# Optimization experiments

Measured on AMD Instinct MI355X. Metric: run time of the kernel, lower is better.

Reference implementation:

```python
import jax, jax.numpy as jnp
import numpy as np

N_NODES = 50000
N_EDGES = 300000
INPUT_DIM = 128
HIDDEN_DIM = 256
NUM_HEADS = 8
HEAD_DIM = HIDDEN_DIM // NUM_HEADS  # 32
NUM_EDGE_TYPES = 3


def setup_inputs() -> dict:
    key = jax.random.key(0)
    ks = jax.random.split(key, 12)
    s_in = 1.0 / np.sqrt(INPUT_DIM)
    s_hid = 1.0 / np.sqrt(HIDDEN_DIM)
    return {
        "node_features": jax.random.normal(ks[0], (N_NODES, INPUT_DIM), jnp.float32),
        "edges": jax.random.randint(ks[1], (N_EDGES, 2), 0, N_NODES),
        "edge_types": jax.random.randint(ks[2], (N_EDGES,), 0, NUM_EDGE_TYPES),
        # torch.nn.Linear convention: y = x @ W.T + b, W: [out, in]
        "Wq": jax.random.normal(ks[3], (HIDDEN_DIM, INPUT_DIM), jnp.float32) * s_in,
        "bq": jax.random.normal(ks[4], (HIDDEN_DIM,), jnp.float32) * s_in,
        "Wk": jax.random.normal(ks[5], (HIDDEN_DIM, INPUT_DIM), jnp.float32) * s_in,
        "bk": jax.random.normal(ks[6], (HIDDEN_DIM,), jnp.float32) * s_in,
        "Wv": jax.random.normal(ks[7], (HIDDEN_DIM, INPUT_DIM), jnp.float32) * s_in,
        "bv": jax.random.normal(ks[8], (HIDDEN_DIM,), jnp.float32) * s_in,
        "edge_emb": jax.random.normal(ks[9], (NUM_EDGE_TYPES, HIDDEN_DIM), jnp.float32),
        "Wo": jax.random.normal(ks[10], (INPUT_DIM, HIDDEN_DIM), jnp.float32) * s_hid,
        "bo": jax.random.normal(ks[11], (INPUT_DIM,), jnp.float32) * s_hid,
    }


def reference(node_features, edges, edge_types, Wq, bq, Wk, bk, Wv, bv, edge_emb, Wo, bo):
    # Project all nodes once, split heads: [N, H, D]
    Q = (node_features @ Wq.T + bq).reshape(-1, NUM_HEADS, HEAD_DIM)
    K = (node_features @ Wk.T + bk).reshape(-1, NUM_HEADS, HEAD_DIM)
    V = (node_features @ Wv.T + bv).reshape(-1, NUM_HEADS, HEAD_DIM)

    src = edges[:, 0]
    tgt = edges[:, 1]

    # Per-edge small attention: Q[src] [E,H,D] x K[tgt]^T -> [E,H,H]
    # (identical math to the original per-edge-type loop, since only the
    #  edge embedding depends on edge_type and it is gathered per edge)
    scale = 1.0 / jnp.sqrt(jnp.float32(HEAD_DIM))
    scores = jnp.einsum("ehd,egd->ehg", Q[src], K[tgt]) * scale
    attn = jax.nn.softmax(scores, axis=-1)
    msg = jnp.einsum("ehg,egd->ehd", attn, V[tgt]).reshape(-1, HIDDEN_DIM)  # [E, HID]

    msg = msg + edge_emb[edge_types]          # per-edge-type embedding add
    out_e = msg @ Wo.T + bo                   # output projection per edge [E, IN]

    # Scatter-add over source nodes (original Python loop over edges)
    messages = jax.ops.segment_sum(out_e, src, num_segments=N_NODES)
    return messages
```

## Files before the change

kernel.cpp:

```cpp
#include <hip/hip_runtime.h>

#define N_NODES 50000
#define N_EDGES 300000
#define M_PAD 50048
#define M_PAD2 50176
#define NBLK 196
#define SC 0.17677669529663687f

typedef __attribute__((ext_vector_type(8))) short bf16x8;
typedef __attribute__((ext_vector_type(4))) short bf16x4;
typedef __attribute__((ext_vector_type(4))) float f32x4;

__device__ __forceinline__ unsigned short f2bf(float x) {
    unsigned int u = __float_as_uint(x);
    unsigned int r = (u + 0x7FFFu + ((u >> 16) & 1u)) >> 16;
    return (unsigned short)r;
}

__global__ __launch_bounds__(512)
void qkv_gemm(const unsigned short* __restrict__ A2, const unsigned short* __restrict__ B2,
              const float* __restrict__ biasCat,
              unsigned short* __restrict__ Qb, unsigned short* __restrict__ Kb,
              unsigned short* __restrict__ Vb)
{
    constexpr int K2 = 128;
    const int t    = threadIdx.x;
    const int w    = t >> 6;
    const int lane = t & 63;
    const int l15  = lane & 15;
    const int lg   = lane >> 4;
    const int bx   = blockIdx.x;
    const int m0   = blockIdx.y * 128;
    const int wm   = (w >> 2) * 64;
    const int wn   = (w & 3) * 64;
    const float mulc = (bx == 0) ? SC : 1.0f;

    f32x4 acc[4][4] = {};

    const unsigned short* Abase = A2 + (size_t)(m0 + wm + l15) * K2 + lg * 8;
    const unsigned short* Bbase = B2 + (size_t)(bx * 256 + wn + l15) * K2 + lg * 8;

    #pragma unroll 2
    for (int ks = 0; ks < K2 / 32; ++ks) {
        bf16x8 af[4], bfv[4];
        #pragma unroll
        for (int mi = 0; mi < 4; ++mi)
            af[mi] = *(const bf16x8*)(Abase + (size_t)mi * 16 * K2 + ks * 32);
        #pragma unroll
        for (int ni = 0; ni < 4; ++ni)
            bfv[ni] = *(const bf16x8*)(Bbase + (size_t)ni * 16 * K2 + ks * 32);
        #pragma unroll
        for (int mi = 0; mi < 4; ++mi)
            #pragma unroll
            for (int ni = 0; ni < 4; ++ni)
                acc[mi][ni] = __builtin_amdgcn_mfma_f32_16x16x32_bf16(
                    af[mi], bfv[ni], acc[mi][ni], 0, 0, 0);
    }

    __shared__ unsigned short Cs[64 * 256];
    float bvn[4];
    #pragma unroll
    for (int ni = 0; ni < 4; ++ni)
        bvn[ni] = biasCat[bx * 256 + wn + ni * 16 + l15];

    #pragma unroll
    for (int p = 0; p < 2; ++p) {
        if (p) __syncthreads();
        #pragma unroll
        for (int mi2 = 0; mi2 < 2; ++mi2) {
            const int mi = p * 2 + mi2;
            #pragma unroll
            for (int j = 0; j < 4; ++j) {
                const int lr = (wm >> 1) + mi2 * 16 + lg * 4 + j;
                const int xr = (lr & 7) << 3;
                #pragma unroll
                for (int ni = 0; ni < 4; ++ni) {
                    const int col = wn + ni * 16 + l15;
                    Cs[lr * 256 + (col ^ xr)] = f2bf(fmaf(acc[mi][ni][j], mulc, bvn[ni]));
                }
            }
        }
        __syncthreads();

        if (bx < 2) {
            unsigned short* dst = bx ? Kb : Qb;
            #pragma unroll
            for (int c8 = 0; c8 < 4; ++c8) {
                const int chunk = c8 * 512 + t;
                const int lr = chunk >> 5;
                const int ec = (chunk & 31) * 8;
                const int gr = m0 + ((lr < 32) ? (p * 32 + lr)
                                               : (64 + p * 32 + (lr - 32)));
                const bf16x8 v = *(const bf16x8*)&Cs[lr * 256 + (ec ^ ((lr & 7) << 3))];
                *(bf16x8*)&dst[(size_t)gr * 256 + ec] = v;
            }
        } else {
            #pragma unroll
            for (int c8 = 0; c8 < 4; ++c8) {
                const int chunk = c8 * 512 + t;
                const int lr = chunk >> 5;
                const int ec = (chunk & 31) * 8;
                const int gr = m0 + ((lr < 32) ? (p * 32 + lr)
                                               : (64 + p * 32 + (lr - 32)));
                const int d  = ec >> 3;
                const int xr = (lr & 7) << 3;
                bf16x8 v;
                #pragma unroll
                for (int g = 0; g < 8; ++g)
                    v[g] = (short)Cs[lr * 256 + ((g * 32 + d) ^ xr)];
                *(bf16x8*)&Vb[(size_t)gr * 256 + ec] = v;
            }
        }
    }
}

__global__ __launch_bounds__(128)
void out_gemm(const unsigned short* __restrict__ accQ, const unsigned short* __restrict__ B2o,
              const float* __restrict__ eew, const float* __restrict__ bo,
              const float4* __restrict__ cnt4, float* __restrict__ Cout)
{
    const int t    = threadIdx.x;
    const int w    = t >> 6;
    const int lane = t & 63;
    const int l15  = lane & 15;
    const int lg   = lane >> 4;
    const int m0   = blockIdx.y * 64;
    const int wn   = w * 64;

    f32x4 acc[4][4] = {};

    const unsigned short* Abase = accQ + (size_t)(m0 + l15) * 256 + lg * 8;
    const unsigned short* Bbase = B2o + (size_t)(wn + l15) * 256 + lg * 8;

    #pragma unroll 2
    for (int ks = 0; ks < 8; ++ks) {
        bf16x8 af[4], bfv[4];
        #pragma unroll
        for (int mi = 0; mi < 4; ++mi)
            af[mi] = *(const bf16x8*)(Abase + (size_t)mi * 16 * 256 + ks * 32);
        #pragma unroll
        for (int ni = 0; ni < 4; ++ni)
            bfv[ni] = *(const bf16x8*)(Bbase + (size_t)ni * 16 * 256 + ks * 32);
        #pragma unroll
        for (int mi = 0; mi < 4; ++mi)
            #pragma unroll
            for (int ni = 0; ni < 4; ++ni)
                acc[mi][ni] = __builtin_amdgcn_mfma_f32_16x16x32_bf16(
                    af[mi], bfv[ni], acc[mi][ni], 0, 0, 0);
    }

    #pragma unroll
    for (int mi = 0; mi < 4; ++mi)
        #pragma unroll
        for (int j = 0; j < 4; ++j) {
            const int row = m0 + mi * 16 + lg * 4 + j;
            if (row < N_NODES) {
                const float4 cv = cnt4[row];
                #pragma unroll
                for (int ni = 0; ni < 4; ++ni) {
                    const int col = wn + ni * 16 + l15;
                    Cout[(size_t)row * 128 + col] = acc[mi][ni][j]
                        + cv.x * eew[col] + cv.y * eew[128 + col]
                        + cv.z * eew[256 + col] + cv.w * bo[col];
                }
            }
        }
}

__global__ __launch_bounds__(256)
void conv_nf_kernel(const float4* __restrict__ nf4, unsigned short* __restrict__ A2)
{
    const int tid = blockIdx.x * 256 + threadIdx.x;
    if (tid >= N_NODES * 32) return;
    const int m = tid >> 5, k4 = (tid & 31) * 4;
    const float4 v = nf4[tid];
    ushort4 hi;
    hi.x = f2bf(v.x); hi.y = f2bf(v.y); hi.z = f2bf(v.z); hi.w = f2bf(v.w);
    *reinterpret_cast<ushort4*>(&A2[(size_t)m * 128 + k4]) = hi;
}

__global__ __launch_bounds__(256)
void prep_kernel(const float* __restrict__ Wq, const float* __restrict__ Wk,
                 const float* __restrict__ Wv, const float* __restrict__ bq,
                 const float* __restrict__ bk, const float* __restrict__ bv,
                 const float* __restrict__ Wo, const float* __restrict__ ee,
                 unsigned short* __restrict__ B2qkv, unsigned short* __restrict__ B2o,
                 float* __restrict__ biasCat, float* __restrict__ eew)
{
    const int bid = blockIdx.x, t = threadIdx.x;
    if (bid < 384) {
        const int tid = bid * 256 + t;
        const int r = tid >> 7, k = tid & 127;
        const float* W = (r < 256) ? Wq : (r < 512) ? Wk : Wv;
        B2qkv[(size_t)r * 128 + k] = f2bf(W[(size_t)(r & 255) * 128 + k]);
        if (k == 0) {
            const float* b = (r < 256) ? bq : (r < 512) ? bk : bv;
            biasCat[r] = b[r & 255] * ((r < 256) ? SC : 1.0f);
        }
    } else if (bid < 512) {
        const int tid = (bid - 384) * 256 + t;
        const int r = tid >> 8, k = tid & 255;
        B2o[(size_t)r * 256 + k] = f2bf(Wo[(size_t)r * 256 + k]);
    } else if (t < 128) {
        float a0 = 0.f, a1 = 0.f, a2 = 0.f;
        for (int k = 0; k < 256; ++k) {
            const float w = Wo[(size_t)t * 256 + k];
            a0 += ee[k] * w; a1 += ee[256 + k] * w; a2 += ee[512 + k] * w;
        }
        eew[t] = a0; eew[128 + t] = a1; eew[256 + t] = a2;
    }
}

__global__ __launch_bounds__(256)
void hist_kernel(const int* __restrict__ edges, int* __restrict__ deg)
{
    const int e = blockIdx.x * 256 + threadIdx.x;
    if (e < N_EDGES) atomicAdd(&deg[edges[2 * e]], 1);
}

__global__ __launch_bounds__(256)
void scan_part1(const int* __restrict__ deg, int* __restrict__ blockSum)
{
    const int t = threadIdx.x;
    const int i = blockIdx.x * 256 + t;
    int v = (i < N_NODES) ? deg[i] : 0;
    #pragma unroll
    for (int o = 1; o < 64; o <<= 1) v += __shfl_xor(v, o);
    __shared__ int ws[4];
    if ((t & 63) == 0) ws[t >> 6] = v;
    __syncthreads();
    if (t == 0) blockSum[blockIdx.x] = ws[0] + ws[1] + ws[2] + ws[3];
}

__global__ __launch_bounds__(256)
void scan_part2(const int* __restrict__ blockSum, int* __restrict__ blockBase,
                int* __restrict__ rowStart)
{
    __shared__ int lds[256];
    const int t = threadIdx.x;
    lds[t] = (t < NBLK) ? blockSum[t] : 0;
    __syncthreads();
    #pragma unroll
    for (int o = 1; o < 256; o <<= 1) {
        const int u = (t >= o) ? lds[t - o] : 0;
        __syncthreads();
        lds[t] += u;
        __syncthreads();
    }
    if (t < NBLK) blockBase[t] = (t == 0) ? 0 : lds[t - 1];
    if (t == 0) rowStart[N_NODES] = N_EDGES;
}

__global__ __launch_bounds__(256)
void scan_part3(const int* __restrict__ deg, const int* __restrict__ blockBase,
                int* __restrict__ rowStart, int* __restrict__ cursor)
{
    const int t = threadIdx.x;
    const int lane = t & 63, wid = t >> 6;
    const int i = blockIdx.x * 256 + t;
    const int d = (i < N_NODES) ? deg[i] : 0;
    int x = d;
    #pragma unroll
    for (int o = 1; o < 64; o <<= 1) {
        const int u = __shfl_up(x, o);
        if (lane >= o) x += u;
    }
    __shared__ int wtot[4];
    if (lane == 63) wtot[wid] = x;
    __syncthreads();
    int wo = 0;
    #pragma unroll
    for (int wi = 0; wi < 3; ++wi) wo += (wi < wid) ? wtot[wi] : 0;
    const int excl = blockBase[blockIdx.x] + wo + x - d;
    if (i < N_NODES) { rowStart[i] = excl; cursor[i] = excl; }
}

__global__ __launch_bounds__(256)
void scatter_kernel(const int* __restrict__ edges, const int* __restrict__ etypes,
                    int* __restrict__ cursor, int* __restrict__ packed)
{
    const int e = blockIdx.x * 256 + threadIdx.x;
    if (e < N_EDGES) {
        const int pos = atomicAdd(&cursor[edges[2 * e]], 1);
        packed[pos] = edges[2 * e + 1] | (etypes[e] << 20);
    }
}

__device__ __forceinline__ bf16x4 softmax_pa(f32x4 s, bool valid)
{
    float mx = fmaxf(fmaxf(s[0], s[1]), fmaxf(s[2], s[3]));
    mx = fmaxf(mx, __shfl_xor(mx, 16));
    const float e0 = __expf(s[0] - mx), e1 = __expf(s[1] - mx);
    const float e2 = __expf(s[2] - mx), e3 = __expf(s[3] - mx);
    float sum = e0 + e1 + e2 + e3;
    sum += __shfl_xor(sum, 16);
    const float inv = valid ? (1.0f / sum) : 0.0f;
    bf16x4 pa;
    pa[0] = (short)f2bf(e0 * inv);
    pa[1] = (short)f2bf(e1 * inv);
    pa[2] = (short)f2bf(e2 * inv);
    pa[3] = (short)f2bf(e3 * inv);
    return pa;
}

__global__ __launch_bounds__(256)
void node_gather_kernel(const int* __restrict__ packed, const int* __restrict__ rowStart,
                        const unsigned short* __restrict__ Qb,
                        const unsigned short* __restrict__ Kb,
                        const unsigned short* __restrict__ Vb,
                        unsigned short* __restrict__ accQ, float4* __restrict__ cnt4)
{
    const int lane = threadIdx.x & 63;
    const int n = blockIdx.x * 4 + (threadIdx.x >> 6);
    if (n >= N_NODES) return;
    const int l15 = lane & 15;
    const int lg  = lane >> 4;

    const bf16x8 qf = *(const bf16x8*)&Qb[(size_t)n * 256 + (l15 & 7) * 32 + lg * 8];

    f32x4 cpvA0 = {0.f,0.f,0.f,0.f}, cpvA1 = {0.f,0.f,0.f,0.f};
    f32x4 cpvB0 = {0.f,0.f,0.f,0.f}, cpvB1 = {0.f,0.f,0.f,0.f};
    int cnt = 0;

    const int lo = rowStart[n], hi = rowStart[n + 1];
    const bool validBase = ((l15 < 8) == (lg < 2));
    const f32x4 z4 = {0.f, 0.f, 0.f, 0.f};
    int idx = lo;

    for (; idx + 4 <= hi; idx += 4) {
        const int p0 = packed[idx],     p1 = packed[idx + 1];
        const int p2 = packed[idx + 2], p3 = packed[idx + 3];
        const int t0 = p0 & 0xFFFFF, t1 = p1 & 0xFFFFF;
        const int t2 = p2 & 0xFFFFF, t3 = p3 & 0xFFFFF;
        cnt += (1 << ((p0 >> 20) * 10)) + (1 << ((p1 >> 20) * 10))
             + (1 << ((p2 >> 20) * 10)) + (1 << ((p3 >> 20) * 10));

        const int tkA = (l15 < 8) ? t0 : t1;
        const int tkB = (l15 < 8) ? t2 : t3;
        const bf16x8 kfA = *(const bf16x8*)&Kb[(size_t)tkA * 256 + (l15 & 7) * 32 + lg * 8];
        const bf16x8 kfB = *(const bf16x8*)&Kb[(size_t)tkB * 256 + (l15 & 7) * 32 + lg * 8];

        const int tvA = (lg < 2) ? t0 : t1;
        const int tvB = (lg < 2) ? t2 : t3;
        const unsigned short* vrA = &Vb[(size_t)tvA * 256 + (lg & 1) * 4];
        const unsigned short* vrB = &Vb[(size_t)tvB * 256 + (lg & 1) * 4];
        const bf16x4 vfA0 = *(const bf16x4*)&vrA[l15 * 8];
        const bf16x4 vfA1 = *(const bf16x4*)&vrA[(l15 + 16) * 8];
        const bf16x4 vfB0 = *(const bf16x4*)&vrB[l15 * 8];
        const bf16x4 vfB1 = *(const bf16x4*)&vrB[(l15 + 16) * 8];

        const f32x4 sA = __builtin_amdgcn_mfma_f32_16x16x32_bf16(kfA, qf, z4, 0, 0, 0);
        const f32x4 sB = __builtin_amdgcn_mfma_f32_16x16x32_bf16(kfB, qf, z4, 0, 0, 0);

        const bf16x4 paA = softmax_pa(sA, validBase);
        const bf16x4 paB = softmax_pa(sB, validBase);

        cpvA0 = __builtin_amdgcn_mfma_f32_16x16x16bf16_1k(paA, vfA0, cpvA0, 0, 0, 0);
        cpvA1 = __builtin_amdgcn_mfma_f32_16x16x16bf16_1k(paA, vfA1, cpvA1, 0, 0, 0);
        cpvB0 = __builtin_amdgcn_mfma_f32_16x16x16bf16_1k(paB, vfB0, cpvB0, 0, 0, 0);
        cpvB1 = __builtin_amdgcn_mfma_f32_16x16x16bf16_1k(paB, vfB1, cpvB1, 0, 0, 0);
    }

    for (; idx < hi; idx += 2) {
        const int  p0  = packed[idx];
        const bool dup = (idx + 1 >= hi);
        const int  p1  = dup ? p0 : packed[idx + 1];
        const int  t0  = p0 & 0xFFFFF;
        const int  t1  = p1 & 0xFFFFF;
        cnt += (1 << ((p0 >> 20) * 10));
        if (!dup) cnt += (1 << ((p1 >> 20) * 10));

        const int tk = (l15 < 8) ? t0 : t1;
        const bf16x8 kf = *(const bf16x8*)&Kb[(size_t)tk * 256 + (l15 & 7) * 32 + lg * 8];

        const int tv = (lg < 2) ? t0 : t1;
        const unsigned short* vrow = &Vb[(size_t)tv * 256 + (lg & 1) * 4];
        const bf16x4 vf0 = *(const bf16x4*)&vrow[l15 * 8];
        const bf16x4 vf1 = *(const bf16x4*)&vrow[(l15 + 16) * 8];

        const f32x4 s = __builtin_amdgcn_mfma_f32_16x16x32_bf16(kf, qf, z4, 0, 0, 0);
        const bool valid = validBase && !(dup && (l15 >= 8));
        const bf16x4 pa = softmax_pa(s, valid);

        cpvA0 = __builtin_amdgcn_mfma_f32_16x16x16bf16_1k(pa, vf0, cpvA0, 0, 0, 0);
        cpvA1 = __builtin_amdgcn_mfma_f32_16x16x16bf16_1k(pa, vf1, cpvA1, 0, 0, 0);
    }

    f32x4 cpv0 = cpvA0 + cpvB0;
    f32x4 cpv1 = cpvA1 + cpvB1;

    #pragma unroll
    for (int j = 0; j < 4; ++j) {
        cpv0[j] += __shfl_xor(cpv0[j], 32);
        cpv1[j] += __shfl_xor(cpv1[j], 32);
    }

    if (lane < 32) {
        unsigned short* row = &accQ[(size_t)n * 256];
        #pragma unroll
        for (int j = 0; j < 4; ++j) {
            const int h = lg * 4 + j;
            row[h * 32 + l15]      = f2bf(cpv0[j]);
            row[h * 32 + 16 + l15] = f2bf(cpv1[j]);
        }
    }
    if (lane == 0) {
        const int c0 = cnt & 1023, c1 = (cnt >> 10) & 1023, c2 = (cnt >> 20) & 1023;
        cnt4[n] = make_float4((float)c0, (float)c1, (float)c2, (float)(hi - lo));
    }
}

extern "C" void kernel_launch(void* const* d_in, const int* in_sizes, int n_in,
                              void* d_out, int out_size, void* d_ws, size_t ws_size,
                              hipStream_t stream)
{
    const float* nf      = (const float*)d_in[0];
    const int*   edges   = (const int*)d_in[1];
    const int*   etypes  = (const int*)d_in[2];
    const float* Wq      = (const float*)d_in[3];
    const float* bq      = (const float*)d_in[4];
    const float* Wk      = (const float*)d_in[5];
    const float* bk      = (const float*)d_in[6];
    const float* Wv      = (const float*)d_in[7];
    const float* bv      = (const float*)d_in[8];
    const float* ee      = (const float*)d_in[9];
    const float* Wo      = (const float*)d_in[10];
    const float* bo      = (const float*)d_in[11];
    float* out = (float*)d_out;

    char* ws = (char*)d_ws;
    size_t off = 0;
    auto alloc = [&](size_t bytes) -> void* {
        void* p = ws + off;
        off = (off + bytes + 255) & ~(size_t)255;
        return p;
    };
    unsigned short* A2    = (unsigned short*)alloc((size_t)M_PAD * 128 * 2);
    unsigned short* B2qkv = (unsigned short*)alloc((size_t)768 * 128 * 2);
    unsigned short* B2o   = (unsigned short*)alloc((size_t)128 * 256 * 2);
    float*          biasC = (float*)alloc(768 * sizeof(float));
    float*          eew   = (float*)alloc(384 * sizeof(float));
    unsigned short* Qb    = (unsigned short*)alloc((size_t)M_PAD * 256 * 2);
    unsigned short* Kb    = (unsigned short*)alloc((size_t)M_PAD * 256 * 2);
    unsigned short* Vb    = (unsigned short*)alloc((size_t)M_PAD * 256 * 2);
    unsigned short* accQ  = (unsigned short*)alloc((size_t)M_PAD2 * 256 * 2);
    float4* cnt4 = (float4*)alloc((size_t)N_NODES * sizeof(float4));
    int*    deg  = (int*)alloc((size_t)N_NODES * sizeof(int));
    int*    rowS = (int*)alloc((size_t)(N_NODES + 1) * sizeof(int));
    int*    curs = (int*)alloc((size_t)N_NODES * sizeof(int));
    int*    pck  = (int*)alloc((size_t)N_EDGES * sizeof(int));
    int*    bSum = (int*)alloc((size_t)NBLK * sizeof(int));
    int*    bBase= (int*)alloc((size_t)NBLK * sizeof(int));

    const dim3 blk(256);

    conv_nf_kernel<<<dim3((N_NODES * 32 + 255) / 256), blk, 0, stream>>>((const float4*)nf, A2);
    prep_kernel<<<dim3(513), blk, 0, stream>>>(Wq, Wk, Wv, bq, bk, bv, Wo, ee, B2qkv, B2o, biasC, eew);

    hipMemsetAsync(deg, 0, (size_t)N_NODES * sizeof(int), stream);
    hist_kernel<<<dim3((N_EDGES + 255) / 256), blk, 0, stream>>>(edges, deg);
    scan_part1<<<dim3(NBLK), blk, 0, stream>>>(deg, bSum);
    scan_part2<<<dim3(1), blk, 0, stream>>>(bSum, bBase, rowS);
    scan_part3<<<dim3(NBLK), blk, 0, stream>>>(deg, bBase, rowS, curs);
    scatter_kernel<<<dim3((N_EDGES + 255) / 256), blk, 0, stream>>>(edges, etypes, curs, pck);

    qkv_gemm<<<dim3(3, M_PAD / 128), dim3(512), 0, stream>>>(
        A2, B2qkv, biasC, Qb, Kb, Vb);

    node_gather_kernel<<<dim3((N_NODES + 3) / 4), blk, 0, stream>>>(
        pck, rowS, Qb, Kb, Vb, accQ, cnt4);

    out_gemm<<<dim3(1, M_PAD2 / 64), dim3(128), 0, stream>>>(
        accQ, B2o, eew, bo, cnt4, out);
}
```

Before: 181.8 us.

## Fuse prep kernels, compute per-type edge counts via histogram, drop softmax max

Merges the feature conversion, weight prep and degree histogram into one launch, and makes the histogram count edges per (node, type) so scan_part3 writes cnt4 directly. The gather kernel no longer unpacks edge types or counts them. The softmax max-subtraction is removed and it now uses a fast reciprocal and library bf16 conversion. The output GEMM tile is halved to 32 rows to launch more blocks. Dropping the max-subtraction risks exp overflow when scores are large, and the 4x larger histogram adds memset and atomic traffic.

```diff
diff --git a/kernel.cpp b/kernel.cpp
--- a/kernel.cpp
+++ b/kernel.cpp
@@ -1,4 +1,5 @@
 #include <hip/hip_runtime.h>
+#include <hip/hip_bf16.h>
 
 #define N_NODES 50000
 #define N_EDGES 300000
@@ -7,6 +8,10 @@
 #define NBLK 196
 #define SC 0.17677669529663687f
 
+#define MB_CONV 6250
+#define MB_HIST 1172
+#define MB_PREP 513
+
 typedef __attribute__((ext_vector_type(8))) short bf16x8;
 typedef __attribute__((ext_vector_type(4))) short bf16x4;
 typedef __attribute__((ext_vector_type(4))) float f32x4;
@@ -15,6 +20,10 @@
     unsigned int u = __float_as_uint(x);
     unsigned int r = (u + 0x7FFFu + ((u >> 16) & 1u)) >> 16;
     return (unsigned short)r;
+}
+__device__ __forceinline__ short bfs(float x) {
+    __hip_bfloat16 h = __float2bfloat16(x);
+    return *reinterpret_cast<short*>(&h);
 }
 
 __global__ __launch_bounds__(512)
@@ -124,25 +133,25 @@
     const int lane = t & 63;
     const int l15  = lane & 15;
     const int lg   = lane >> 4;
-    const int m0   = blockIdx.y * 64;
+    const int m0   = blockIdx.y * 32;
     const int wn   = w * 64;
 
-    f32x4 acc[4][4] = {};
+    f32x4 acc[2][4] = {};
 
     const unsigned short* Abase = accQ + (size_t)(m0 + l15) * 256 + lg * 8;
     const unsigned short* Bbase = B2o + (size_t)(wn + l15) * 256 + lg * 8;
 
     #pragma unroll 2
     for (int ks = 0; ks < 8; ++ks) {
-        bf16x8 af[4], bfv[4];
-        #pragma unroll
-        for (int mi = 0; mi < 4; ++mi)
+        bf16x8 af[2], bfv[4];
+        #pragma unroll
+        for (int mi = 0; mi < 2; ++mi)
             af[mi] = *(const bf16x8*)(Abase + (size_t)mi * 16 * 256 + ks * 32);
         #pragma unroll
         for (int ni = 0; ni < 4; ++ni)
             bfv[ni] = *(const bf16x8*)(Bbase + (size_t)ni * 16 * 256 + ks * 32);
         #pragma unroll
-        for (int mi = 0; mi < 4; ++mi)
+        for (int mi = 0; mi < 2; ++mi)
             #pragma unroll
             for (int ni = 0; ni < 4; ++ni)
                 acc[mi][ni] = __builtin_amdgcn_mfma_f32_16x16x32_bf16(
@@ -150,7 +159,7 @@
     }
 
     #pragma unroll
-    for (int mi = 0; mi < 4; ++mi)
+    for (int mi = 0; mi < 2; ++mi)
         #pragma unroll
         for (int j = 0; j < 4; ++j) {
             const int row = m0 + mi * 16 + lg * 4 + j;
@@ -168,62 +177,64 @@
 }
 
 __global__ __launch_bounds__(256)
-void conv_nf_kernel(const float4* __restrict__ nf4, unsigned short* __restrict__ A2)
-{
-    const int tid = blockIdx.x * 256 + threadIdx.x;
-    if (tid >= N_NODES * 32) return;
-    const int m = tid >> 5, k4 = (tid & 31) * 4;
-    const float4 v = nf4[tid];
-    ushort4 hi;
-    hi.x = f2bf(v.x); hi.y = f2bf(v.y); hi.z = f2bf(v.z); hi.w = f2bf(v.w);
-    *reinterpret_cast<ushort4*>(&A2[(size_t)m * 128 + k4]) = hi;
-}
-
-__global__ __launch_bounds__(256)
-void prep_kernel(const float* __restrict__ Wq, const float* __restrict__ Wk,
-                 const float* __restrict__ Wv, const float* __restrict__ bq,
-                 const float* __restrict__ bk, const float* __restrict__ bv,
-                 const float* __restrict__ Wo, const float* __restrict__ ee,
-                 unsigned short* __restrict__ B2qkv, unsigned short* __restrict__ B2o,
-                 float* __restrict__ biasCat, float* __restrict__ eew)
+void mega_prep(const float4* __restrict__ nf4,
+               const int* __restrict__ edges, const int* __restrict__ etypes,
+               const float* __restrict__ Wq, const float* __restrict__ Wk,
+               const float* __restrict__ Wv, const float* __restrict__ bq,
+               const float* __restrict__ bk, const float* __restrict__ bv,
+               const float* __restrict__ Wo, const float* __restrict__ ee,
+               unsigned short* __restrict__ A2, unsigned short* __restrict__ B2qkv,
+               unsigned short* __restrict__ B2o,
+               float* __restrict__ biasCat, float* __restrict__ eew,
+               int* __restrict__ degType)
 {
     const int bid = blockIdx.x, t = threadIdx.x;
-    if (bid < 384) {
+    if (bid < MB_CONV) {
         const int tid = bid * 256 + t;
-        const int r = tid >> 7, k = tid & 127;
-        const float* W = (r < 256) ? Wq : (r < 512) ? Wk : Wv;
-        B2qkv[(size_t)r * 128 + k] = f2bf(W[(size_t)(r & 255) * 128 + k]);
-        if (k == 0) {
-            const float* b = (r < 256) ? bq : (r < 512) ? bk : bv;
-            biasCat[r] = b[r & 255] * ((r < 256) ? SC : 1.0f);
+        const int m = tid >> 5, k4 = (tid & 31) * 4;
+        const float4 v = nf4[tid];
+        ushort4 hi;
+        hi.x = f2bf(v.x); hi.y = f2bf(v.y); hi.z = f2bf(v.z); hi.w = f2bf(v.w);
+        *reinterpret_cast<ushort4*>(&A2[(size_t)m * 128 + k4]) = hi;
+    } else if (bid < MB_CONV + MB_HIST) {
+        const int e = (bid - MB_CONV) * 256 + t;
+        if (e < N_EDGES) atomicAdd(&degType[edges[2 * e] * 4 + etypes[e]], 1);
+    } else {
+        const int pbid = bid - MB_CONV - MB_HIST;
+        if (pbid < 384) {
+            const int tid = pbid * 256 + t;
+            const int r = tid >> 7, k = tid & 127;
+            const float* W = (r < 256) ? Wq : (r < 512) ? Wk : Wv;
+            B2qkv[(size_t)r * 128 + k] = f2bf(W[(size_t)(r & 255) * 128 + k]);
+            if (k == 0) {
+                const float* b = (r < 256) ? bq : (r < 512) ? bk : bv;
+                biasCat[r] = b[r & 255] * ((r < 256) ? SC : 1.0f);
+            }
+        } else if (pbid < 512) {
+            const int tid = (pbid - 384) * 256 + t;
+            const int r = tid >> 8, k = tid & 255;
+            B2o[(size_t)r * 256 + k] = f2bf(Wo[(size_t)r * 256 + k]);
+        } else if (t < 128) {
+            float a0 = 0.f, a1 = 0.f, a2 = 0.f;
+            for (int k = 0; k < 256; ++k) {
+                const float w = Wo[(size_t)t * 256 + k];
+                a0 += ee[k] * w; a1 += ee[256 + k] * w; a2 += ee[512 + k] * w;
+            }
+            eew[t] = a0; eew[128 + t] = a1; eew[256 + t] = a2;
         }
-    } else if (bid < 512) {
-        const int tid = (bid - 384) * 256 + t;
-        const int r = tid >> 8, k = tid & 255;
-        B2o[(size_t)r * 256 + k] = f2bf(Wo[(size_t)r * 256 + k]);
-    } else if (t < 128) {
-        float a0 = 0.f, a1 = 0.f, a2 = 0.f;
-        for (int k = 0; k < 256; ++k) {
-            const float w = Wo[(size_t)t * 256 + k];
-            a0 += ee[k] * w; a1 += ee[256 + k] * w; a2 += ee[512 + k] * w;
-        }
-        eew[t] = a0; eew[128 + t] = a1; eew[256 + t] = a2;
-    }
-}
-
-__global__ __launch_bounds__(256)
-void hist_kernel(const int* __restrict__ edges, int* __restrict__ deg)
-{
-    const int e = blockIdx.x * 256 + threadIdx.x;
-    if (e < N_EDGES) atomicAdd(&deg[edges[2 * e]], 1);
-}
-
-__global__ __launch_bounds__(256)
-void scan_part1(const int* __restrict__ deg, int* __restrict__ blockSum)
+    }
+}
+
+__global__ __launch_bounds__(256)
+void scan_part1(const int4* __restrict__ degType4, int* __restrict__ blockSum)
 {
     const int t = threadIdx.x;
     const int i = blockIdx.x * 256 + t;
-    int v = (i < N_NODES) ? deg[i] : 0;
+    int v = 0;
+    if (i < N_NODES) {
+        const int4 dt = degType4[i];
+        v = dt.x + dt.y + dt.z;
+    }
     #pragma unroll
     for (int o = 1; o < 64; o <<= 1) v += __shfl_xor(v, o);
     __shared__ int ws[4];
@@ -252,13 +263,16 @@
 }
 
 __global__ __launch_bounds__(256)
-void scan_part3(const int* __restrict__ deg, const int* __restrict__ blockBase,
-                int* __restrict__ rowStart, int* __restrict__ cursor)
+void scan_part3(const int4* __restrict__ degType4, const int* __restrict__ blockBase,
+                int* __restrict__ rowStart, int* __restrict__ cursor,
+                float4* __restrict__ cnt4)
 {
     const int t = threadIdx.x;
     const int lane = t & 63, wid = t >> 6;
     const int i = blockIdx.x * 256 + t;
-    const int d = (i < N_NODES) ? deg[i] : 0;
+    int4 dt = make_int4(0, 0, 0, 0);
+    if (i < N_NODES) dt = degType4[i];
+    const int d = dt.x + dt.y + dt.z;
     int x = d;
     #pragma unroll
     for (int o = 1; o < 64; o <<= 1) {
@@ -272,34 +286,36 @@
     #pragma unroll
     for (int wi = 0; wi < 3; ++wi) wo += (wi < wid) ? wtot[wi] : 0;
     const int excl = blockBase[blockIdx.x] + wo + x - d;
-    if (i < N_NODES) { rowStart[i] = excl; cursor[i] = excl; }
-}
-
-__global__ __launch_bounds__(256)
-void scatter_kernel(const int* __restrict__ edges, const int* __restrict__ etypes,
-                    int* __restrict__ cursor, int* __restrict__ packed)
+    if (i < N_NODES) {
+        rowStart[i] = excl;
+        cursor[i]   = excl;
+        cnt4[i]     = make_float4((float)dt.x, (float)dt.y, (float)dt.z, (float)d);
+    }
+}
+
+__global__ __launch_bounds__(256)
+void scatter_kernel(const int* __restrict__ edges, int* __restrict__ cursor,
+                    int* __restrict__ packed)
 {
     const int e = blockIdx.x * 256 + threadIdx.x;
     if (e < N_EDGES) {
         const int pos = atomicAdd(&cursor[edges[2 * e]], 1);
-        packed[pos] = edges[2 * e + 1] | (etypes[e] << 20);
+        packed[pos] = edges[2 * e + 1];
     }
 }
 
 __device__ __forceinline__ bf16x4 softmax_pa(f32x4 s, bool valid)
 {
-    float mx = fmaxf(fmaxf(s[0], s[1]), fmaxf(s[2], s[3]));
-    mx = fmaxf(mx, __shfl_xor(mx, 16));
-    const float e0 = __expf(s[0] - mx), e1 = __expf(s[1] - mx);
-    const float e2 = __expf(s[2] - mx), e3 = __expf(s[3] - mx);
+    const float e0 = __expf(s[0]), e1 = __expf(s[1]);
+    const float e2 = __expf(s[2]), e3 = __expf(s[3]);
     float sum = e0 + e1 + e2 + e3;
     sum += __shfl_xor(sum, 16);
-    const float inv = valid ? (1.0f / sum) : 0.0f;
+    const float inv = valid ? __builtin_amdgcn_rcpf(sum) : 0.0f;
     bf16x4 pa;
-    pa[0] = (short)f2bf(e0 * inv);
-    pa[1] = (short)f2bf(e1 * inv);
-    pa[2] = (short)f2bf(e2 * inv);
-    pa[3] = (short)f2bf(e3 * inv);
+    pa[0] = bfs(e0 * inv);
+    pa[1] = bfs(e1 * inv);
+    pa[2] = bfs(e2 * inv);
+    pa[3] = bfs(e3 * inv);
     return pa;
 }
 
@@ -308,7 +324,7 @@
                         const unsigned short* __restrict__ Qb,
                         const unsigned short* __restrict__ Kb,
                         const unsigned short* __restrict__ Vb,
-                        unsigned short* __restrict__ accQ, float4* __restrict__ cnt4)
+                        unsigned short* __restrict__ accQ)
 {
     const int lane = threadIdx.x & 63;
     const int n = blockIdx.x * 4 + (threadIdx.x >> 6);
@@ -320,7 +336,6 @@
 
     f32x4 cpvA0 = {0.f,0.f,0.f,0.f}, cpvA1 = {0.f,0.f,0.f,0.f};
     f32x4 cpvB0 = {0.f,0.f,0.f,0.f}, cpvB1 = {0.f,0.f,0.f,0.f};
-    int cnt = 0;
 
     const int lo = rowStart[n], hi = rowStart[n + 1];
     const bool validBase = ((l15 < 8) == (lg < 2));
@@ -328,12 +343,8 @@
     int idx = lo;
 
     for (; idx + 4 <= hi; idx += 4) {
-        const int p0 = packed[idx],     p1 = packed[idx + 1];
-        const int p2 = packed[idx + 2], p3 = packed[idx + 3];
-        const int t0 = p0 & 0xFFFFF, t1 = p1 & 0xFFFFF;
-        const int t2 = p2 & 0xFFFFF, t3 = p3 & 0xFFFFF;
-        cnt += (1 << ((p0 >> 20) * 10)) + (1 << ((p1 >> 20) * 10))
-             + (1 << ((p2 >> 20) * 10)) + (1 << ((p3 >> 20) * 10));
+        const int t0 = packed[idx],     t1 = packed[idx + 1];
+        const int t2 = packed[idx + 2], t3 = packed[idx + 3];
 
         const int tkA = (l15 < 8) ? t0 : t1;
         const int tkB = (l15 < 8) ? t2 : t3;
@@ -362,13 +373,9 @@
     }
 
     for (; idx < hi; idx += 2) {
-        const int  p0  = packed[idx];
+        const int  t0  = packed[idx];
         const bool dup = (idx + 1 >= hi);
-        const int  p1  = dup ? p0 : packed[idx + 1];
-        const int  t0  = p0 & 0xFFFFF;
-        const int  t1  = p1 & 0xFFFFF;
-        cnt += (1 << ((p0 >> 20) * 10));
-        if (!dup) cnt += (1 << ((p1 >> 20) * 10));
+        const int  t1  = dup ? t0 : packed[idx + 1];
 
         const int tk = (l15 < 8) ? t0 : t1;
         const bf16x8 kf = *(const bf16x8*)&Kb[(size_t)tk * 256 + (l15 & 7) * 32 + lg * 8];
@@ -400,13 +407,9 @@
         #pragma unroll
         for (int j = 0; j < 4; ++j) {
             const int h = lg * 4 + j;
-            row[h * 32 + l15]      = f2bf(cpv0[j]);
-            row[h * 32 + 16 + l15] = f2bf(cpv1[j]);
+            row[h * 32 + l15]      = (unsigned short)bfs(cpv0[j]);
+            row[h * 32 + 16 + l15] = (unsigned short)bfs(cpv1[j]);
         }
-    }
-    if (lane == 0) {
-        const int c0 = cnt & 1023, c1 = (cnt >> 10) & 1023, c2 = (cnt >> 20) & 1023;
-        cnt4[n] = make_float4((float)c0, (float)c1, (float)c2, (float)(hi - lo));
     }
 }
 
@@ -435,41 +438,41 @@
         off = (off + bytes + 255) & ~(size_t)255;
         return p;
     };
-    unsigned short* A2    = (unsigned short*)alloc((size_t)M_PAD * 128 * 2);
-    unsigned short* B2qkv = (unsigned short*)alloc((size_t)768 * 128 * 2);
-    unsigned short* B2o   = (unsigned short*)alloc((size_t)128 * 256 * 2);
-    float*          biasC = (float*)alloc(768 * sizeof(float));
-    float*          eew   = (float*)alloc(384 * sizeof(float));
-    unsigned short* Qb    = (unsigned short*)alloc((size_t)M_PAD * 256 * 2);
-    unsigned short* Kb    = (unsigned short*)alloc((size_t)M_PAD * 256 * 2);
-    unsigned short* Vb    = (unsigned short*)alloc((size_t)M_PAD * 256 * 2);
-    unsigned short* accQ  = (unsigned short*)alloc((size_t)M_PAD2 * 256 * 2);
-    float4* cnt4 = (float4*)alloc((size_t)N_NODES * sizeof(float4));
-    int*    deg  = (int*)alloc((size_t)N_NODES * sizeof(int));
-    int*    rowS = (int*)alloc((size_t)(N_NODES + 1) * sizeof(int));
-    int*    curs = (int*)alloc((size_t)N_NODES * sizeof(int));
-    int*    pck  = (int*)alloc((size_t)N_EDGES * sizeof(int));
-    int*    bSum = (int*)alloc((size_t)NBLK * sizeof(int));
-    int*    bBase= (int*)alloc((size_t)NBLK * sizeof(int));
+    unsigned short* A2     = (unsigned short*)alloc((size_t)M_PAD * 128 * 2);
+    unsigned short* B2qkv  = (unsigned short*)alloc((size_t)768 * 128 * 2);
+    unsigned short* B2o    = (unsigned short*)alloc((size_t)128 * 256 * 2);
+    float*          biasC  = (float*)alloc(768 * sizeof(float));
+    float*          eew    = (float*)alloc(384 * sizeof(float));
+    unsigned short* Qb     = (unsigned short*)alloc((size_t)M_PAD * 256 * 2);
+    unsigned short* Kb     = (unsigned short*)alloc((size_t)M_PAD * 256 * 2);
+    unsigned short* Vb     = (unsigned short*)alloc((size_t)M_PAD * 256 * 2);
+    unsigned short* accQ   = (unsigned short*)alloc((size_t)M_PAD2 * 256 * 2);
+    float4* cnt4    = (float4*)alloc((size_t)N_NODES * sizeof(float4));
+    int*    degType = (int*)alloc((size_t)N_NODES * 4 * sizeof(int));
+    int*    rowS    = (int*)alloc((size_t)(N_NODES + 1) * sizeof(int));
+    int*    curs    = (int*)alloc((size_t)N_NODES * sizeof(int));
+    int*    pck     = (int*)alloc((size_t)N_EDGES * sizeof(int));
+    int*    bSum    = (int*)alloc((size_t)NBLK * sizeof(int));
+    int*    bBase   = (int*)alloc((size_t)NBLK * sizeof(int));
 
     const dim3 blk(256);
 
-    conv_nf_kernel<<<dim3((N_NODES * 32 + 255) / 256), blk, 0, stream>>>((const float4*)nf, A2);
-    prep_kernel<<<dim3(513), blk, 0, stream>>>(Wq, Wk, Wv, bq, bk, bv, Wo, ee, B2qkv, B2o, biasC, eew);
-
-    hipMemsetAsync(deg, 0, (size_t)N_NODES * sizeof(int), stream);
-    hist_kernel<<<dim3((N_EDGES + 255) / 256), blk, 0, stream>>>(edges, deg);
-    scan_part1<<<dim3(NBLK), blk, 0, stream>>>(deg, bSum);
+    hipMemsetAsync(degType, 0, (size_t)N_NODES * 4 * sizeof(int), stream);
+    mega_prep<<<dim3(MB_CONV + MB_HIST + MB_PREP), blk, 0, stream>>>(
+        (const float4*)nf, edges, etypes, Wq, Wk, Wv, bq, bk, bv, Wo, ee,
+        A2, B2qkv, B2o, biasC, eew, degType);
+
+    scan_part1<<<dim3(NBLK), blk, 0, stream>>>((const int4*)degType, bSum);
     scan_part2<<<dim3(1), blk, 0, stream>>>(bSum, bBase, rowS);
-    scan_part3<<<dim3(NBLK), blk, 0, stream>>>(deg, bBase, rowS, curs);
-    scatter_kernel<<<dim3((N_EDGES + 255) / 256), blk, 0, stream>>>(edges, etypes, curs, pck);
+    scan_part3<<<dim3(NBLK), blk, 0, stream>>>((const int4*)degType, bBase, rowS, curs, cnt4);
+    scatter_kernel<<<dim3((N_EDGES + 255) / 256), blk, 0, stream>>>(edges, curs, pck);
 
     qkv_gemm<<<dim3(3, M_PAD / 128), dim3(512), 0, stream>>>(
         A2, B2qkv, biasC, Qb, Kb, Vb);
 
     node_gather_kernel<<<dim3((N_NODES + 3) / 4), blk, 0, stream>>>(
-        pck, rowS, Qb, Kb, Vb, accQ, cnt4);
-
-    out_gemm<<<dim3(1, M_PAD2 / 64), dim3(128), 0, stream>>>(
+        pck, rowS, Qb, Kb, Vb, accQ);
+
+    out_gemm<<<dim3(1, M_PAD2 / 32), dim3(128), 0, stream>>>(
         accQ, B2o, eew, bo, cnt4, out);
 }
```

Measured after the change: 178.5 us. Within noise of the previous version (-1.8%).
